# Kernel optimization log

Measured on AMD Instinct MI355X. Metric: run time of the kernel, lower is better.

The kernel has to match this reference:

```python
import jax, jax.numpy as jnp
import numpy as np

N = 100000      # num nodes
E = 1600000     # num edges (avg degree 16)
ND = 32         # node_dim
ED = 32         # edge_dim
OD = 32         # out_dim


def setup_inputs() -> dict:
    key = jax.random.key(0)
    ks = jax.random.split(key, 7)
    node_x = jax.random.normal(ks[0], (N, ND), dtype=jnp.float32)
    edge_x = jax.random.normal(ks[1], (E, ED), dtype=jnp.float32)
    # forward() initializes g.ndata['z'] = torch.rand(N, node_dim+edge_dim)
    z_init = jax.random.uniform(ks[2], (N, ND + ED), dtype=jnp.float32)
    # pre_layer: Linear(ND+ED -> ND+ED); update_layer: Linear(2*ND+ED -> OD)
    W_pre = jax.random.normal(ks[3], (ND + ED, ND + ED), dtype=jnp.float32) / np.sqrt(ND + ED)
    b_pre = jnp.zeros((ND + ED,), dtype=jnp.float32)
    W_upd = jax.random.normal(ks[4], (2 * ND + ED, OD), dtype=jnp.float32) / np.sqrt(2 * ND + ED)
    b_upd = jnp.zeros((OD,), dtype=jnp.float32)
    src = jax.random.randint(ks[5], (E,), 0, N, dtype=jnp.int32)
    dst = jax.random.randint(ks[6], (E,), 0, N, dtype=jnp.int32)
    return {"node_x": node_x, "edge_x": edge_x, "z_init": z_init,
            "W_pre": W_pre, "b_pre": b_pre, "W_upd": W_upd, "b_upd": b_upd,
            "src": src, "dst": dst}


def reference(node_x, edge_x, z_init, W_pre, b_pre, W_upd, b_upd, src, dst):
    n = node_x.shape[0]
    # msg_func: per-edge gather + concat + Linear. Messages depend only on the
    # STATIC node feature 'x', so DGL's topological propagation is equivalent
    # to one edge-parallel pass.
    msg = jnp.concatenate([node_x[src], edge_x], axis=1) @ W_pre + b_pre  # [E, ND+ED]
    # reduce_func: sum over mailbox + ReLU (only fires for nodes with in-edges;
    # nodes with no incoming edges keep the random z_init).
    agg = jax.ops.segment_sum(msg, dst, num_segments=n)                    # [N, ND+ED]
    deg = jax.ops.segment_sum(jnp.ones_like(dst, dtype=node_x.dtype), dst, num_segments=n)
    z = jnp.where((deg > 0)[:, None], jax.nn.relu(agg), z_init)           # [N, ND+ED]
    # node_update: concat + Linear + ReLU
    h = jax.nn.relu(jnp.concatenate([node_x, z], axis=1) @ W_upd + b_upd)  # [N, OD]
    return h
```

## Files before the change

### kernel.cpp

```cpp
#include <hip/hip_runtime.h>


#define N_NODES 100000
#define N_EDGES 1600000
#define ND 32
#define ED 32
#define OD 32
#define ZD 64
#define NTILE 98

__device__ inline float bcast(float v, int lane) {
    return __uint_as_float(__builtin_amdgcn_readlane(__float_as_uint(v), lane));
}

__global__ __launch_bounds__(256) void hist(const int* __restrict__ dst,
                                            int* __restrict__ cnt) {
    int e = blockIdx.x * 256 + threadIdx.x;
    if (e < N_EDGES) atomicAdd(&cnt[dst[e]], 1);
}

__global__ __launch_bounds__(1024) void scan_part(const int* __restrict__ cnt,
                                                  int* __restrict__ part) {
    __shared__ int s[1024];
    int i = blockIdx.x * 1024 + threadIdx.x;
    s[threadIdx.x] = (i < N_NODES) ? cnt[i] : 0;
    __syncthreads();
    for (int off = 512; off > 0; off >>= 1) {
        if (threadIdx.x < off) s[threadIdx.x] += s[threadIdx.x + off];
        __syncthreads();
    }
    if (threadIdx.x == 0) part[blockIdx.x] = s[0];
}

__global__ void scan_top(int* part) {
    __shared__ int s[128];
    int v = (threadIdx.x < NTILE) ? part[threadIdx.x] : 0;
    s[threadIdx.x] = v;
    __syncthreads();
    for (int off = 1; off < 128; off <<= 1) {
        int u = (threadIdx.x >= off) ? s[threadIdx.x - off] : 0;
        __syncthreads();
        s[threadIdx.x] += u;
        __syncthreads();
    }
    if (threadIdx.x < NTILE) part[threadIdx.x] = s[threadIdx.x] - v;
}

__global__ __launch_bounds__(1024) void scan_local(const int* __restrict__ cnt,
                                                   const int* __restrict__ part,
                                                   int* __restrict__ cursor) {
    __shared__ int s[1024];
    int i = blockIdx.x * 1024 + threadIdx.x;
    int v = (i < N_NODES) ? cnt[i] : 0;
    s[threadIdx.x] = v;
    __syncthreads();
    for (int off = 1; off < 1024; off <<= 1) {
        int u = (threadIdx.x >= off) ? s[threadIdx.x - off] : 0;
        __syncthreads();
        s[threadIdx.x] += u;
        __syncthreads();
    }
    if (i < N_NODES) cursor[i] = part[blockIdx.x] + s[threadIdx.x] - v;
}

__global__ __launch_bounds__(256) void permute_ids(
    const int* __restrict__ src, const int* __restrict__ dst,
    int* __restrict__ cursor, int2* __restrict__ pair)
{
    int e = blockIdx.x * 256 + threadIdx.x;
    if (e >= N_EDGES) return;
    int pos = atomicAdd(&cursor[dst[e]], 1);
    pair[pos] = make_int2(src[e], e);
}

__global__ __launch_bounds__(256, 1) void z_csr(
    const float* __restrict__ node_x, const float* __restrict__ edge_x,
    const float* __restrict__ z_init,
    const float* __restrict__ W_pre, const float* __restrict__ b_pre,
    const int* __restrict__ cnt, const int* __restrict__ cursor,
    const int2* __restrict__ pair, float* __restrict__ zbuf)
{
    const int l = threadIdx.x & 63;
    float Wp[ZD];
    #pragma unroll
    for (int k = 0; k < ZD; ++k) Wp[k] = W_pre[k * ZD + l];
    const float bp = b_pre[l];

    int w  = (blockIdx.x * 256 + threadIdx.x) >> 6;
    int nw = (gridDim.x * 256) >> 6;
    for (int n = w; n < N_NODES; n += nw) {
        int dg = cnt[n];
        float z;
        if (dg > 0) {
            int end = cursor[n];
            int j = end - dg;
            float acc = 0.0f;
            for (; j + 4 <= end; j += 4) {
                int2 p0 = pair[j], p1 = pair[j+1], p2 = pair[j+2], p3 = pair[j+3];
                float v0 = (l < ND) ? node_x[(long)p0.x * ND + l]
                                    : edge_x[(long)p0.y * ED + (l - ND)];
                float v1 = (l < ND) ? node_x[(long)p1.x * ND + l]
                                    : edge_x[(long)p1.y * ED + (l - ND)];
                float v2 = (l < ND) ? node_x[(long)p2.x * ND + l]
                                    : edge_x[(long)p2.y * ED + (l - ND)];
                float v3 = (l < ND) ? node_x[(long)p3.x * ND + l]
                                    : edge_x[(long)p3.y * ED + (l - ND)];
                acc += v0 + v1 + v2 + v3;
            }
            for (; j < end; ++j) {
                int2 p0 = pair[j];
                acc += (l < ND) ? node_x[(long)p0.x * ND + l]
                                : edge_x[(long)p0.y * ED + (l - ND)];
            }
            float a0 = (float)dg * bp, a1 = 0.0f;
            #pragma unroll
            for (int k = 0; k < ZD; k += 2) {
                a0 += bcast(acc, k)     * Wp[k];
                a1 += bcast(acc, k + 1) * Wp[k + 1];
            }
            z = fmaxf(a0 + a1, 0.0f);
        } else {
            z = z_init[(long)n * ZD + l];
        }
        zbuf[(long)n * ZD + l] = z;
    }
}

__global__ __launch_bounds__(256) void edge_scatter(
    const float* __restrict__ node_x, const float* __restrict__ edge_x,
    const int* __restrict__ src, const int* __restrict__ dst,
    float* __restrict__ S, int* __restrict__ degI)
{
    long t = (long)blockIdx.x * 256 + threadIdx.x;
    int e = (int)(t >> 6), l = (int)(t & 63);
    if (e >= N_EDGES) return;
    int s = src[e], d = dst[e];
    float v = (l < ND) ? node_x[(long)s * ND + l] : edge_x[(long)e * ED + (l - ND)];
    atomicAdd(&S[(long)d * ZD + l], v);
    if (l == 0) atomicAdd(&degI[d], 1);
}

__global__ __launch_bounds__(256, 1) void z_dense(
    const float* __restrict__ z_init,
    const float* __restrict__ W_pre, const float* __restrict__ b_pre,
    float* __restrict__ S, const int* __restrict__ degI)
{
    const int l = threadIdx.x & 63;
    float Wp[ZD];
    #pragma unroll
    for (int k = 0; k < ZD; ++k) Wp[k] = W_pre[k * ZD + l];
    const float bp = b_pre[l];
    int w  = (blockIdx.x * 256 + threadIdx.x) >> 6;
    int nw = (gridDim.x * 256) >> 6;
    for (int n = w; n < N_NODES; n += nw) {
        int dg = degI[n];
        float sv = S[(long)n * ZD + l];
        float z;
        if (dg > 0) {
            float a0 = (float)dg * bp, a1 = 0.0f;
            #pragma unroll
            for (int k = 0; k < ZD; k += 2) {
                a0 += bcast(sv, k)     * Wp[k];
                a1 += bcast(sv, k + 1) * Wp[k + 1];
            }
            z = fmaxf(a0 + a1, 0.0f);
        } else {
            z = z_init[(long)n * ZD + l];
        }
        S[(long)n * ZD + l] = z;
    }
}

__global__ __launch_bounds__(256, 1) void h_upd(
    const float* __restrict__ node_x,
    const float* __restrict__ W_upd, const float* __restrict__ b_upd,
    const float* __restrict__ zbuf, float* __restrict__ out)
{
    const int l = threadIdx.x & 63;
    const int c = l & 31;
    float Wu[ND + ZD];
    #pragma unroll
    for (int k = 0; k < ND + ZD; ++k) Wu[k] = W_upd[k * OD + c];
    const float bu = b_upd[c];
    int w  = (blockIdx.x * 256 + threadIdx.x) >> 6;
    int nw = (gridDim.x * 256) >> 6;
    for (int n = w; n < N_NODES; n += nw) {
        float zv = zbuf[(long)n * ZD + l];
        float xv = node_x[(long)n * ND + c];
        float h0 = bu, h1 = 0.0f;
        #pragma unroll
        for (int k = 0; k < ND; k += 2) {
            h0 += bcast(xv, k)     * Wu[k];
            h1 += bcast(xv, k + 1) * Wu[k + 1];
        }
        #pragma unroll
        for (int k = 0; k < ZD; k += 2) {
            h0 += bcast(zv, k)     * Wu[ND + k];
            h1 += bcast(zv, k + 1) * Wu[ND + k + 1];
        }
        if (l < OD) out[(long)n * OD + l] = fmaxf(h0 + h1, 0.0f);
    }
}

extern "C" void kernel_launch(void* const* d_in, const int* in_sizes, int n_in,
                              void* d_out, int out_size, void* d_ws, size_t ws_size,
                              hipStream_t stream)
{
    const float* node_x = (const float*)d_in[0];
    const float* edge_x = (const float*)d_in[1];
    const float* z_init = (const float*)d_in[2];
    const float* W_pre  = (const float*)d_in[3];
    const float* b_pre  = (const float*)d_in[4];
    const float* W_upd  = (const float*)d_in[5];
    const float* b_upd  = (const float*)d_in[6];
    const int*   src    = (const int*)d_in[7];
    const int*   dst    = (const int*)d_in[8];
    float* out = (float*)d_out;

    size_t need = (size_t)N_EDGES * sizeof(int2)
                + (size_t)N_NODES * ZD * sizeof(float)
                + ((size_t)2 * N_NODES + 128) * sizeof(int);

    if (ws_size >= need) {
        int2*  pair   = (int2*)d_ws;
        float* zbuf   = (float*)(pair + N_EDGES);
        int*   cnt    = (int*)(zbuf + (size_t)N_NODES * ZD);
        int*   part   = cnt + N_NODES;
        int*   cursor = part + 128;

        (void)hipMemsetAsync(cnt, 0, N_NODES * sizeof(int), stream);
        hist<<<(N_EDGES + 255) / 256, 256, 0, stream>>>(dst, cnt);
        scan_part<<<NTILE, 1024, 0, stream>>>(cnt, part);
        scan_top<<<1, 128, 0, stream>>>(part);
        scan_local<<<NTILE, 1024, 0, stream>>>(cnt, part, cursor);
        permute_ids<<<(N_EDGES + 255) / 256, 256, 0, stream>>>(src, dst, cursor, pair);
        z_csr<<<2048, 256, 0, stream>>>(node_x, edge_x, z_init, W_pre, b_pre,
                                        cnt, cursor, pair, zbuf);
        h_upd<<<2048, 256, 0, stream>>>(node_x, W_upd, b_upd, zbuf, out);
    } else {
        float* S    = (float*)d_ws;
        int*   degI = (int*)(S + (size_t)N_NODES * ZD);
        (void)hipMemsetAsync(d_ws, 0,
            ((size_t)N_NODES * ZD + N_NODES) * sizeof(float), stream);
        edge_scatter<<<(int)(((long)N_EDGES * 64 + 255) / 256), 256, 0, stream>>>(
            node_x, edge_x, src, dst, S, degI);
        z_dense<<<2048, 256, 0, stream>>>(z_init, W_pre, b_pre, S, degI);
        h_upd<<<2048, 256, 0, stream>>>(node_x, W_upd, b_upd, S, out);
    }
}
```

Measured before the change: 724.3 us.

## Privatize histogram and cursor atomics into 8 copies; unroll CSR gather by 8

The degree histogram and the permutation cursors are split into 8 private copies chosen by block index. A reduce kernel sums the copies, and a new kernel builds per-copy starting offsets. This spreads out atomic contention on hot dst entries, at the cost of extra memset, reduce and offset passes over 8x-sized arrays. The z_csr gather loop is unrolled to 8 edges using a unified base pointer and 32-bit index math, which adds memory-level parallelism. cursor now holds segment starts rather than ends.

```diff
diff --git a/kernel.cpp b/kernel.cpp
--- a/kernel.cpp
+++ b/kernel.cpp
@@ -13,10 +13,22 @@
     return __uint_as_float(__builtin_amdgcn_readlane(__float_as_uint(v), lane));
 }
 
-__global__ __launch_bounds__(256) void hist(const int* __restrict__ dst,
-                                            int* __restrict__ cnt) {
+__global__ __launch_bounds__(256) void hist8(const int* __restrict__ dst,
+                                             int* __restrict__ h8) {
     int e = blockIdx.x * 256 + threadIdx.x;
-    if (e < N_EDGES) atomicAdd(&cnt[dst[e]], 1);
+    if (e < N_EDGES)
+        atomicAdd(&h8[(blockIdx.x & 7) * N_NODES + dst[e]], 1);
+}
+
+__global__ __launch_bounds__(256) void reduce8(const int* __restrict__ h8,
+                                               int* __restrict__ cnt) {
+    int n = blockIdx.x * 256 + threadIdx.x;
+    if (n < N_NODES) {
+        int s = 0;
+        #pragma unroll
+        for (int x = 0; x < 8; ++x) s += h8[x * N_NODES + n];
+        cnt[n] = s;
+    }
 }
 
 __global__ __launch_bounds__(1024) void scan_part(const int* __restrict__ cnt,
@@ -63,13 +75,27 @@
     if (i < N_NODES) cursor[i] = part[blockIdx.x] + s[threadIdx.x] - v;
 }
 
+__global__ __launch_bounds__(256) void build_cur8(const int* __restrict__ h8,
+                                                  const int* __restrict__ cursor,
+                                                  int* __restrict__ c8) {
+    int n = blockIdx.x * 256 + threadIdx.x;
+    if (n < N_NODES) {
+        int run = cursor[n];
+        #pragma unroll
+        for (int x = 0; x < 8; ++x) {
+            c8[x * N_NODES + n] = run;
+            run += h8[x * N_NODES + n];
+        }
+    }
+}
+
 __global__ __launch_bounds__(256) void permute_ids(
     const int* __restrict__ src, const int* __restrict__ dst,
-    int* __restrict__ cursor, int2* __restrict__ pair)
+    int* __restrict__ c8, int2* __restrict__ pair)
 {
     int e = blockIdx.x * 256 + threadIdx.x;
     if (e >= N_EDGES) return;
-    int pos = atomicAdd(&cursor[dst[e]], 1);
+    int pos = atomicAdd(&c8[(blockIdx.x & 7) * N_NODES + dst[e]], 1);
     pair[pos] = make_int2(src[e], e);
 }
 
@@ -85,6 +111,7 @@
     #pragma unroll
     for (int k = 0; k < ZD; ++k) Wp[k] = W_pre[k * ZD + l];
     const float bp = b_pre[l];
+    const float* __restrict__ gbase = (l < ND) ? node_x : (edge_x - ND);
 
     int w  = (blockIdx.x * 256 + threadIdx.x) >> 6;
     int nw = (gridDim.x * 256) >> 6;
@@ -92,25 +119,34 @@
         int dg = cnt[n];
         float z;
         if (dg > 0) {
-            int end = cursor[n];
-            int j = end - dg;
+            int j = cursor[n];
+            int end = j + dg;
             float acc = 0.0f;
-            for (; j + 4 <= end; j += 4) {
-                int2 p0 = pair[j], p1 = pair[j+1], p2 = pair[j+2], p3 = pair[j+3];
-                float v0 = (l < ND) ? node_x[(long)p0.x * ND + l]
-                                    : edge_x[(long)p0.y * ED + (l - ND)];
-                float v1 = (l < ND) ? node_x[(long)p1.x * ND + l]
-                                    : edge_x[(long)p1.y * ED + (l - ND)];
-                float v2 = (l < ND) ? node_x[(long)p2.x * ND + l]
-                                    : edge_x[(long)p2.y * ED + (l - ND)];
-                float v3 = (l < ND) ? node_x[(long)p3.x * ND + l]
-                                    : edge_x[(long)p3.y * ED + (l - ND)];
-                acc += v0 + v1 + v2 + v3;
+            for (; j + 8 <= end; j += 8) {
+                int2 p0 = pair[j],   p1 = pair[j+1], p2 = pair[j+2], p3 = pair[j+3];
+                int2 p4 = pair[j+4], p5 = pair[j+5], p6 = pair[j+6], p7 = pair[j+7];
+                int s0 = (l < ND) ? p0.x : p0.y;
+                int s1 = (l < ND) ? p1.x : p1.y;
+                int s2 = (l < ND) ? p2.x : p2.y;
+                int s3 = (l < ND) ? p3.x : p3.y;
+                int s4 = (l < ND) ? p4.x : p4.y;
+                int s5 = (l < ND) ? p5.x : p5.y;
+                int s6 = (l < ND) ? p6.x : p6.y;
+                int s7 = (l < ND) ? p7.x : p7.y;
+                float v0 = gbase[(unsigned)s0 * 32u + (unsigned)l];
+                float v1 = gbase[(unsigned)s1 * 32u + (unsigned)l];
+                float v2 = gbase[(unsigned)s2 * 32u + (unsigned)l];
+                float v3 = gbase[(unsigned)s3 * 32u + (unsigned)l];
+                float v4 = gbase[(unsigned)s4 * 32u + (unsigned)l];
+                float v5 = gbase[(unsigned)s5 * 32u + (unsigned)l];
+                float v6 = gbase[(unsigned)s6 * 32u + (unsigned)l];
+                float v7 = gbase[(unsigned)s7 * 32u + (unsigned)l];
+                acc += ((v0 + v1) + (v2 + v3)) + ((v4 + v5) + (v6 + v7));
             }
             for (; j < end; ++j) {
                 int2 p0 = pair[j];
-                acc += (l < ND) ? node_x[(long)p0.x * ND + l]
-                                : edge_x[(long)p0.y * ED + (l - ND)];
+                int s0 = (l < ND) ? p0.x : p0.y;
+                acc += gbase[(unsigned)s0 * 32u + (unsigned)l];
             }
             float a0 = (float)dg * bp, a1 = 0.0f;
             #pragma unroll
@@ -219,7 +255,7 @@
 
     size_t need = (size_t)N_EDGES * sizeof(int2)
                 + (size_t)N_NODES * ZD * sizeof(float)
-                + ((size_t)2 * N_NODES + 128) * sizeof(int);
+                + ((size_t)18 * N_NODES + 128) * sizeof(int);
 
     if (ws_size >= need) {
         int2*  pair   = (int2*)d_ws;
@@ -227,13 +263,17 @@
         int*   cnt    = (int*)(zbuf + (size_t)N_NODES * ZD);
         int*   part   = cnt + N_NODES;
         int*   cursor = part + 128;
-
-        (void)hipMemsetAsync(cnt, 0, N_NODES * sizeof(int), stream);
-        hist<<<(N_EDGES + 255) / 256, 256, 0, stream>>>(dst, cnt);
+        int*   h8     = cursor + N_NODES;
+        int*   c8     = h8 + 8 * N_NODES;
+
+        (void)hipMemsetAsync(h8, 0, 8 * N_NODES * sizeof(int), stream);
+        hist8<<<(N_EDGES + 255) / 256, 256, 0, stream>>>(dst, h8);
+        reduce8<<<(N_NODES + 255) / 256, 256, 0, stream>>>(h8, cnt);
         scan_part<<<NTILE, 1024, 0, stream>>>(cnt, part);
         scan_top<<<1, 128, 0, stream>>>(part);
         scan_local<<<NTILE, 1024, 0, stream>>>(cnt, part, cursor);
-        permute_ids<<<(N_EDGES + 255) / 256, 256, 0, stream>>>(src, dst, cursor, pair);
+        build_cur8<<<(N_NODES + 255) / 256, 256, 0, stream>>>(h8, cursor, c8);
+        permute_ids<<<(N_EDGES + 255) / 256, 256, 0, stream>>>(src, dst, c8, pair);
         z_csr<<<2048, 256, 0, stream>>>(node_x, edge_x, z_init, W_pre, b_pre,
                                         cnt, cursor, pair, zbuf);
         h_upd<<<2048, 256, 0, stream>>>(node_x, W_upd, b_upd, zbuf, out);
```

Result: faster. 680.8 us (-6.0%).
